# Kernel optimization log

Measured on AMD Instinct MI355X. Metric: run time of the kernel, lower is better.

The kernel has to match this reference:

```python
import jax, jax.numpy as jnp
import numpy as np


def _local_patches(x, patch_size):
    """Zero-padded sliding patches, matching F.unfold semantics.
    x: [N, C, H, W] -> [N, C, P*P, H, W] (window positions row-major,
    same per-channel ordering as unfold's C*P*P channel layout)."""
    N, C, H, W = x.shape
    pad = patch_size // 2
    xp = jnp.pad(x, ((0, 0), (0, 0), (pad, pad), (pad, pad)))
    views = [xp[:, :, i:i + H, j:j + W]
             for i in range(patch_size) for j in range(patch_size)]
    return jnp.stack(views, axis=2)  # [N, C, P*P, H, W]


def setup_inputs() -> dict:
    key = jax.random.key(0)
    x_lab = jax.random.normal(key, (16, 3, 512, 512), dtype=jnp.float32)
    return {"x_lab": x_lab, "patch_size": 3, "alpha": 1, "scale_factor": 1}


def reference(x_lab, patch_size, alpha, scale_factor):
    # scale_factor == 1 -> F.interpolate is the identity (nearest, scale 1).
    patches = _local_patches(x_lab, patch_size)       # [N, 3, P*P, H, W]
    local_l = patches[:, 0]                            # [N, P*P, H, W]
    local_a = patches[:, 1]
    local_b = patches[:, 2]
    l = x_lab[:, 0:1]                                  # [N, 1, H, W]
    local_difference = (local_l - l) ** 2
    correlation = jax.nn.softmax(-local_difference / alpha, axis=1)
    wa = jnp.sum(correlation * local_a, axis=1, keepdims=True)
    wb = jnp.sum(correlation * local_b, axis=1, keepdims=True)
    return jnp.concatenate([wa, wb], axis=1)           # [N, 2, H, W]
```

## Files before the change

### kernel.cpp

```cpp
#include <hip/hip_runtime.h>

#define NB   16
#define HH   512
#define WW   512
#define HWSZ (HH * WW)

__global__ __launch_bounds__(256) void WeightedAverage_kernel(
    const float* __restrict__ x,
    const int*   __restrict__ alpha_p,
    float*       __restrict__ out)
{
    int idx = blockIdx.x * 256 + threadIdx.x;
    int w = idx & (WW - 1);
    int h = (idx >> 9) & (HH - 1);
    int n = idx >> 18;

    const float inv_alpha = 1.0f / (float)(*alpha_p);

    const float* Lp = x + (size_t)n * 3 * HWSZ;
    const float* Ap = Lp + HWSZ;
    const float* Bp = Lp + 2 * HWSZ;

    int c = h * WW + w;
    float l = Lp[c];

    float den = 0.0f, na = 0.0f, nb = 0.0f;

#pragma unroll
    for (int dy = -1; dy <= 1; ++dy) {
        int hh = h + dy;
        bool rowv = ((unsigned)hh < (unsigned)HH);
#pragma unroll
        for (int dx = -1; dx <= 1; ++dx) {
            int ww = w + dx;
            bool v = rowv && ((unsigned)ww < (unsigned)WW);
            int o = hh * WW + ww;
            float lv = v ? Lp[o] : 0.0f;
            float av = v ? Ap[o] : 0.0f;
            float bv = v ? Bp[o] : 0.0f;
            float d  = lv - l;
            float wt = __expf(-d * d * inv_alpha);
            den += wt;
            na  += wt * av;
            nb  += wt * bv;
        }
    }

    float r = 1.0f / den;
    float* o0 = out + (size_t)n * 2 * HWSZ + c;
    o0[0]    = na * r;
    o0[HWSZ] = nb * r;
}

extern "C" void kernel_launch(void* const* d_in, const int* in_sizes, int n_in,
                              void* d_out, int out_size, void* d_ws, size_t ws_size,
                              hipStream_t stream) {
    const float* x     = (const float*)d_in[0];
    const int*   alpha = (const int*)d_in[2];
    float*       out   = (float*)d_out;

    int total_pixels = NB * HWSZ;
    dim3 grid(total_pixels / 256);
    WeightedAverage_kernel<<<grid, 256, 0, stream>>>(x, alpha, out);
}
```

Measured before the change: 111.9 us.

## Process four pixels per thread with float4 loads and wavefront-shuffle halos

Each thread now computes four adjacent output pixels, loading each of the three neighbouring rows for L, A and B as float4. Left and right halo values come from neighbouring lanes via shuffles, with global loads only at wavefront edges. The centre tap skips its exponential, weights use exp2 with a prescaled constant, the division becomes a hardware reciprocal, and outputs are stored as float4. This removes redundant scalar loads and per-pixel address math, at the cost of higher register use and slightly lower reciprocal precision.

New measurement: 113.4 us. About the same (+1.3%).

```diff
diff --git a/kernel.cpp b/kernel.cpp
--- a/kernel.cpp
+++ b/kernel.cpp
@@ -5,51 +5,83 @@
 #define WW   512
 #define HWSZ (HH * WW)
 
+__device__ __forceinline__ void load_row6(const float* __restrict__ p, long base,
+                                          bool rowv, bool ledge, bool redge,
+                                          int lane, float v[6]) {
+    float4 c;
+    if (rowv) c = *(const float4*)(p + base);
+    else      c = make_float4(0.f, 0.f, 0.f, 0.f);
+    float lw = __shfl_up(c.w, 1);
+    float rx = __shfl_down(c.x, 1);
+    if (lane == 0)  lw = (ledge || !rowv) ? 0.0f : p[base - 1];
+    if (lane == 63) rx = (redge || !rowv) ? 0.0f : p[base + 4];
+    v[0] = lw; v[1] = c.x; v[2] = c.y; v[3] = c.z; v[4] = c.w; v[5] = rx;
+}
+
 __global__ __launch_bounds__(256) void WeightedAverage_kernel(
     const float* __restrict__ x,
     const int*   __restrict__ alpha_p,
     float*       __restrict__ out)
 {
-    int idx = blockIdx.x * 256 + threadIdx.x;
-    int w = idx & (WW - 1);
-    int h = (idx >> 9) & (HH - 1);
-    int n = idx >> 18;
+    int g    = blockIdx.x * 256 + threadIdx.x;
+    int lane = threadIdx.x & 63;
+    int col  = (g & 127) << 2;
+    int h    = (g >> 7) & 511;
+    int n    = g >> 16;
+    bool ledge = (col == 0);
+    bool redge = (col + 4 == WW);
 
-    const float inv_alpha = 1.0f / (float)(*alpha_p);
+    float m = -1.4426950408889634f / (float)(*alpha_p);
 
     const float* Lp = x + (size_t)n * 3 * HWSZ;
     const float* Ap = Lp + HWSZ;
     const float* Bp = Lp + 2 * HWSZ;
 
-    int c = h * WW + w;
-    float l = Lp[c];
+    float Lr[3][6];
+    long rb[3];
+    bool rv[3];
+#pragma unroll
+    for (int i = 0; i < 3; ++i) {
+        int r = h - 1 + i;
+        rv[i] = ((unsigned)r < (unsigned)HH);
+        rb[i] = (long)r * WW + col;
+        load_row6(Lp, rb[i], rv[i], ledge, redge, lane, Lr[i]);
+    }
 
-    float den = 0.0f, na = 0.0f, nb = 0.0f;
+    float l[4] = { Lr[1][1], Lr[1][2], Lr[1][3], Lr[1][4] };
+    float den[4] = {0.f,0.f,0.f,0.f};
+    float na[4]  = {0.f,0.f,0.f,0.f};
+    float nb[4]  = {0.f,0.f,0.f,0.f};
 
 #pragma unroll
-    for (int dy = -1; dy <= 1; ++dy) {
-        int hh = h + dy;
-        bool rowv = ((unsigned)hh < (unsigned)HH);
+    for (int i = 0; i < 3; ++i) {
+        float Ar[6], Br[6];
+        load_row6(Ap, rb[i], rv[i], ledge, redge, lane, Ar);
+        load_row6(Bp, rb[i], rv[i], ledge, redge, lane, Br);
 #pragma unroll
-        for (int dx = -1; dx <= 1; ++dx) {
-            int ww = w + dx;
-            bool v = rowv && ((unsigned)ww < (unsigned)WW);
-            int o = hh * WW + ww;
-            float lv = v ? Lp[o] : 0.0f;
-            float av = v ? Ap[o] : 0.0f;
-            float bv = v ? Bp[o] : 0.0f;
-            float d  = lv - l;
-            float wt = __expf(-d * d * inv_alpha);
-            den += wt;
-            na  += wt * av;
-            nb  += wt * bv;
+        for (int dx = 0; dx < 3; ++dx) {
+#pragma unroll
+            for (int j = 0; j < 4; ++j) {
+                float d  = Lr[i][j + dx] - l[j];
+                float wt = (i == 1 && dx == 1) ? 1.0f : exp2f(d * d * m);
+                den[j] += wt;
+                na[j]  += wt * Ar[j + dx];
+                nb[j]  += wt * Br[j + dx];
+            }
         }
     }
 
-    float r = 1.0f / den;
-    float* o0 = out + (size_t)n * 2 * HWSZ + c;
-    o0[0]    = na * r;
-    o0[HWSZ] = nb * r;
+    float4 oa, ob;
+    float r0 = __builtin_amdgcn_rcpf(den[0]);
+    float r1 = __builtin_amdgcn_rcpf(den[1]);
+    float r2 = __builtin_amdgcn_rcpf(den[2]);
+    float r3 = __builtin_amdgcn_rcpf(den[3]);
+    oa = make_float4(na[0]*r0, na[1]*r1, na[2]*r2, na[3]*r3);
+    ob = make_float4(nb[0]*r0, nb[1]*r1, nb[2]*r2, nb[3]*r3);
+
+    float* op = out + (size_t)n * 2 * HWSZ + (size_t)h * WW + col;
+    *(float4*)(op)        = oa;
+    *(float4*)(op + HWSZ) = ob;
 }
 
 extern "C" void kernel_launch(void* const* d_in, const int* in_sizes, int n_in,
@@ -59,7 +91,7 @@
     const int*   alpha = (const int*)d_in[2];
     float*       out   = (float*)d_out;
 
-    int total_pixels = NB * HWSZ;
-    dim3 grid(total_pixels / 256);
+    int groups = NB * HWSZ / 4;
+    dim3 grid(groups / 256);
     WeightedAverage_kernel<<<grid, 256, 0, stream>>>(x, alpha, out);
 }
```
